# Kernel optimization log

Hardware: AMD Instinct MI355X
Metric: run time of the kernel (lower is better)

Reference implementation:

```python
import jax, jax.numpy as jnp
import numpy as np

N_NODES = 50000
N_EDGES = 500000
D_IN = 128
D_HID = 128
OUTPUT_DIM = 10.0


def gcn_conv(x, src, dst, edge_weight, W, b, n_nodes):
    # PyG GCNConv: out = D^{-1/2} (A + I) D^{-1/2} X W + b, self-loop weight 1
    xw = x @ W  # [N, D_out]
    # degree at target nodes, including self-loop weight 1
    deg = jax.ops.segment_sum(edge_weight, dst, num_segments=n_nodes) + 1.0
    dinv = jnp.where(deg > 0, jax.lax.rsqrt(deg), 0.0)  # [N]
    norm = dinv[src] * edge_weight * dinv[dst]  # [E]
    msgs = xw[src] * norm[:, None]  # [E, D_out] gathered+scaled messages
    agg = jax.ops.segment_sum(msgs, dst, num_segments=n_nodes)
    # analytic self-loop contribution: norm_ii = dinv_i * 1 * dinv_i
    agg = agg + xw * (dinv * dinv)[:, None]
    return agg + b


def setup_inputs() -> dict:
    key = jax.random.key(0)
    k = jax.random.split(key, 8)
    x = jax.random.normal(k[0], (N_NODES, D_IN), dtype=jnp.float32)
    edge_index = jax.random.randint(k[1], (2, N_EDGES), 0, N_NODES, dtype=jnp.int64)
    edge_weight = jax.random.uniform(k[2], (N_EDGES,), dtype=jnp.float32)
    s1 = 1.0 / np.sqrt(D_IN)
    s2 = 1.0 / np.sqrt(D_HID)
    W1 = jax.random.uniform(k[3], (D_IN, D_HID), minval=-s1, maxval=s1, dtype=jnp.float32)
    b1 = jnp.zeros((D_HID,), dtype=jnp.float32)
    W2 = jax.random.uniform(k[4], (D_HID, D_HID), minval=-s2, maxval=s2, dtype=jnp.float32)
    b2 = jnp.zeros((D_HID,), dtype=jnp.float32)
    Wf = jax.random.uniform(k[5], (D_HID, 1), minval=-s2, maxval=s2, dtype=jnp.float32)
    bf = jax.random.uniform(k[6], (1,), minval=-s2, maxval=s2, dtype=jnp.float32)
    return {"x": x, "edge_index": edge_index, "edge_weight": edge_weight,
            "W1": W1, "b1": b1, "W2": W2, "b2": b2, "Wf": Wf, "bf": bf}


def reference(x, edge_index, edge_weight, W1, b1, W2, b2, Wf, bf):
    src, dst = edge_index[0], edge_index[1]
    h = gcn_conv(x, src, dst, edge_weight, W1, b1, N_NODES)
    h = gcn_conv(h, src, dst, edge_weight, W2, b2, N_NODES)
    out = h @ Wf + bf  # [N, 1]
    return jax.nn.sigmoid(out) * OUTPUT_DIM
```

## Files before the change

### kernel.cpp

```cpp
#include <hip/hip_runtime.h>

#define N_NODES 50000
#define N_EDGES 500000
#define NQ (N_EDGES / 4)
#define D 128
#define NBUCK 196
#define BN 256
#define REG 4096
#define FXS 4194304.0f
#define AXS 2097152.0f

typedef unsigned long long u64;

__global__ void prep_kernel(const float* __restrict__ W1, const float* __restrict__ W2,
                            const float* __restrict__ b1, const float* __restrict__ b2,
                            const float* __restrict__ Wf, const float* __restrict__ bf,
                            float* __restrict__ v, float* __restrict__ consts,
                            unsigned* __restrict__ alloc) {
    const int t = threadIdx.x;
    if (blockIdx.x == 1) {
        if (t < 256) alloc[t] = 0u;
        return;
    }
    __shared__ float u[D];
    if (t < D) {
        float a = 0.f;
#pragma unroll 8
        for (int j = 0; j < D; ++j) a += W2[t * D + j] * Wf[j];
        u[t] = a;
    }
    __syncthreads();
    if (t < D) {
        float a = 0.f;
#pragma unroll 8
        for (int k = 0; k < D; ++k) a += W1[t * D + k] * u[k];
        v[t] = a;
    }
    if (t == 0) {
        float c = 0.f;
        for (int k = 0; k < D; ++k) c += b1[k] * u[k];
        consts[0] = c;
    } else if (t == 1) {
        float c = bf[0];
        for (int k = 0; k < D; ++k) c += b2[k] * Wf[k];
        consts[1] = c;
    }
}

__global__ __launch_bounds__(512) void bucket_kernel(const int* __restrict__ src,
                                                     const int* __restrict__ dst,
                                                     const float* __restrict__ ew,
                                                     unsigned* __restrict__ alloc,
                                                     u64* __restrict__ recs) {
    __shared__ unsigned hist[NBUCK];
    const int t = threadIdx.x;
    if (t < NBUCK) hist[t] = 0u;
    __syncthreads();
    const int q0 = blockIdx.x * 1024 + t;
    const int q1 = q0 + 512;
    int4 dA, sA, dB, sB; float4 wA, wB;
    const bool aA = q0 < NQ, aB = q1 < NQ;
    if (aA) {
        dA = ((const int4*)dst)[q0]; sA = ((const int4*)src)[q0]; wA = ((const float4*)ew)[q0];
        atomicAdd(&hist[dA.x >> 8], 1u); atomicAdd(&hist[dA.y >> 8], 1u);
        atomicAdd(&hist[dA.z >> 8], 1u); atomicAdd(&hist[dA.w >> 8], 1u);
    }
    if (aB) {
        dB = ((const int4*)dst)[q1]; sB = ((const int4*)src)[q1]; wB = ((const float4*)ew)[q1];
        atomicAdd(&hist[dB.x >> 8], 1u); atomicAdd(&hist[dB.y >> 8], 1u);
        atomicAdd(&hist[dB.z >> 8], 1u); atomicAdd(&hist[dB.w >> 8], 1u);
    }
    __syncthreads();
    if (t < NBUCK) hist[t] = atomicAdd(&alloc[t], hist[t]);
    __syncthreads();
#define PLACE(dd, ss, ww)                                                        \
    {   int bkt = (dd) >> 8;                                                     \
        unsigned p = atomicAdd(&hist[bkt], 1u);                                  \
        if (p < REG)                                                             \
            recs[(size_t)bkt * REG + p] =                                        \
                ((u64)__float_as_uint(ww) << 32) |                               \
                ((unsigned)((dd) & 255) << 16) | (unsigned)(ss);                 \
    }
    if (aA) { PLACE(dA.x, sA.x, wA.x) PLACE(dA.y, sA.y, wA.y)
              PLACE(dA.z, sA.z, wA.z) PLACE(dA.w, sA.w, wA.w) }
    if (aB) { PLACE(dB.x, sB.x, wB.x) PLACE(dB.y, sB.y, wB.y)
              PLACE(dB.z, sB.z, wB.z) PLACE(dB.w, sB.w, wB.w) }
#undef PLACE
}

__global__ void gemv_kernel(const float* __restrict__ x, const float* __restrict__ v,
                            float* __restrict__ traw) {
    __shared__ float vs[D];
    const int t = threadIdx.x;
    if (t < D) vs[t] = v[t];
    __syncthreads();
    const int l = t & 31;
    const int n = blockIdx.x * 8 + (t >> 5);
    float4 xv = ((const float4*)(x + (size_t)n * D))[l];
    float a = xv.x * vs[l * 4] + xv.y * vs[l * 4 + 1] +
              xv.z * vs[l * 4 + 2] + xv.w * vs[l * 4 + 3];
#pragma unroll
    for (int off = 16; off > 0; off >>= 1) a += __shfl_xor(a, off);
    if (l == 0) traw[n] = a;
}

__global__ __launch_bounds__(512) void degtw_kernel(const u64* __restrict__ recs,
                                                    const unsigned* __restrict__ alloc,
                                                    const float* __restrict__ traw,
                                                    float* __restrict__ dinv,
                                                    float* __restrict__ tw) {
    __shared__ unsigned ws[BN];
    const int b = blockIdx.x, t = threadIdx.x;
    if (t < BN) ws[t] = 0u;
    __syncthreads();
    unsigned total = alloc[b];
    if (total > REG) total = REG;
    const u64* rb = recs + (size_t)b * REG;
    for (unsigned i = t; i < total; i += 512) {
        u64 r = rb[i];
        float w = __uint_as_float((unsigned)(r >> 32));
        atomicAdd(&ws[((unsigned)r >> 16) & 0xffu], __float2uint_rn(w * FXS));
    }
    __syncthreads();
    if (t < BN) {
        int n = b * BN + t;
        if (n < N_NODES) {
            float di = rsqrtf((float)ws[t] * (1.0f / FXS) + 1.0f);
            dinv[n] = di;
            tw[n] = di * traw[n];
        }
    }
}

__global__ __launch_bounds__(512) void gather_s_kernel(const u64* __restrict__ recs,
                                                       const unsigned* __restrict__ alloc,
                                                       const float* __restrict__ tw,
                                                       const float* __restrict__ dinv,
                                                       const float* __restrict__ consts,
                                                       float* __restrict__ sw) {
    __shared__ int acc[BN];
    const int b = blockIdx.x, t = threadIdx.x;
    if (t < BN) acc[t] = 0;
    __syncthreads();
    unsigned total = alloc[b];
    if (total > REG) total = REG;
    const u64* rb = recs + (size_t)b * REG;
    for (unsigned i = t; i < total; i += 512) {
        u64 r = rb[i];
        unsigned lo = (unsigned)r;
        float m = __uint_as_float((unsigned)(r >> 32)) * tw[lo & 0xffffu];
        atomicAdd(&acc[(lo >> 16) & 0xffu], __float2int_rn(m * AXS));
    }
    __syncthreads();
    if (t < BN) {
        int n = b * BN + t;
        if (n < N_NODES) {
            float di = dinv[n];
            float a = (float)acc[t] * (1.0f / AXS);
            sw[n] = di * (di * (a + tw[n]) + consts[0]);
        }
    }
}

__global__ __launch_bounds__(512) void gather_z_kernel(const u64* __restrict__ recs,
                                                       const unsigned* __restrict__ alloc,
                                                       const float* __restrict__ sw,
                                                       const float* __restrict__ dinv,
                                                       const float* __restrict__ consts,
                                                       float* __restrict__ out) {
    __shared__ int acc[BN];
    const int b = blockIdx.x, t = threadIdx.x;
    if (t < BN) acc[t] = 0;
    __syncthreads();
    unsigned total = alloc[b];
    if (total > REG) total = REG;
    const u64* rb = recs + (size_t)b * REG;
    for (unsigned i = t; i < total; i += 512) {
        u64 r = rb[i];
        unsigned lo = (unsigned)r;
        float m = __uint_as_float((unsigned)(r >> 32)) * sw[lo & 0xffffu];
        atomicAdd(&acc[(lo >> 16) & 0xffu], __float2int_rn(m * AXS));
    }
    __syncthreads();
    if (t < BN) {
        int n = b * BN + t;
        if (n < N_NODES) {
            float di = dinv[n];
            float a = (float)acc[t] * (1.0f / AXS);
            float z = di * (a + sw[n]) + consts[1];
            out[n] = 10.0f / (1.0f + expf(-z));
        }
    }
}

extern "C" void kernel_launch(void* const* d_in, const int* in_sizes, int n_in,
                              void* d_out, int out_size, void* d_ws, size_t ws_size,
                              hipStream_t stream) {
    const float* x  = (const float*)d_in[0];
    const int*   ei = (const int*)d_in[1];
    const float* ew = (const float*)d_in[2];
    const float* W1 = (const float*)d_in[3];
    const float* b1 = (const float*)d_in[4];
    const float* W2 = (const float*)d_in[5];
    const float* b2 = (const float*)d_in[6];
    const float* Wf = (const float*)d_in[7];
    const float* bf = (const float*)d_in[8];
    const int* srcv = ei;
    const int* dstv = ei + N_EDGES;
    float* out = (float*)d_out;

    char* p = (char*)d_ws;
    auto alloc_ws = [&](size_t bytes) { void* r = (void*)p; p += (bytes + 255) & ~(size_t)255; return r; };
    unsigned* alloc  = (unsigned*)alloc_ws(256 * 4);
    u64*      recs   = (u64*)alloc_ws((size_t)NBUCK * REG * 8);
    float*    traw   = (float*)alloc_ws(N_NODES * 4);
    float*    dinv   = (float*)alloc_ws(N_NODES * 4);
    float*    tw     = (float*)alloc_ws(N_NODES * 4);
    float*    sw     = (float*)alloc_ws(N_NODES * 4);
    float*    v      = (float*)alloc_ws(D * 4);
    float*    consts = (float*)alloc_ws(2 * 4);

    const int BB = (NQ + 1023) / 1024;

    prep_kernel<<<2, 256, 0, stream>>>(W1, W2, b1, b2, Wf, bf, v, consts, alloc);

    bucket_kernel<<<BB, 512, 0, stream>>>(srcv, dstv, ew, alloc, recs);

    gemv_kernel<<<N_NODES / 8, 256, 0, stream>>>(x, v, traw);

    degtw_kernel<<<NBUCK, 512, 0, stream>>>(recs, alloc, traw, dinv, tw);
    gather_s_kernel<<<NBUCK, 512, 0, stream>>>(recs, alloc, tw, dinv, consts, sw);
    gather_z_kernel<<<NBUCK, 512, 0, stream>>>(recs, alloc, sw, dinv, consts, out);
}
```

Measured before the change: 118.8 us.

## Replace global-atomic bucketing with per-block cells and fuse kernels into four launches

The bucket layout changes from one global region per destination bucket, filled through global atomic offsets, to fixed 64-slot cells per (bucket, block) with per-cell counts. This removes the global alloc counters, the histogram pass and the prep launch. The prep work moves into an extra block of the build kernel, and the GEMV is merged with the degree computation into one launch. The tw buffer is dropped by computing dinv*traw inside the gather. The risk is cell overflow: edges past 64 per cell are silently dropped, which the test's random uniform distribution makes unlikely but does not rule out.

```diff
diff --git a/kernel.cpp b/kernel.cpp
--- a/kernel.cpp
+++ b/kernel.cpp
@@ -6,180 +6,188 @@
 #define D 128
 #define NBUCK 196
 #define BN 256
-#define REG 4096
+#define NBLK 123
+#define CELL 64
+#define GEMVB 3125
 #define FXS 4194304.0f
 #define AXS 2097152.0f
 
 typedef unsigned long long u64;
 
-__global__ void prep_kernel(const float* __restrict__ W1, const float* __restrict__ W2,
-                            const float* __restrict__ b1, const float* __restrict__ b2,
-                            const float* __restrict__ Wf, const float* __restrict__ bf,
-                            float* __restrict__ v, float* __restrict__ consts,
-                            unsigned* __restrict__ alloc) {
+__global__ __launch_bounds__(512) void build_kernel(const int* __restrict__ src,
+                                                    const int* __restrict__ dst,
+                                                    const float* __restrict__ ew,
+                                                    const float* __restrict__ W1,
+                                                    const float* __restrict__ W2,
+                                                    const float* __restrict__ b1,
+                                                    const float* __restrict__ b2,
+                                                    const float* __restrict__ Wf,
+                                                    const float* __restrict__ bf,
+                                                    u64* __restrict__ recs,
+                                                    unsigned* __restrict__ cnts,
+                                                    float* __restrict__ v,
+                                                    float* __restrict__ consts) {
     const int t = threadIdx.x;
-    if (blockIdx.x == 1) {
-        if (t < 256) alloc[t] = 0u;
+    const int blk = blockIdx.x;
+    if (blk == NBLK) {
+        __shared__ float u[D];
+        if (t < D) {
+            float a = 0.f;
+#pragma unroll 8
+            for (int j = 0; j < D; ++j) a += W2[t * D + j] * Wf[j];
+            u[t] = a;
+        }
+        __syncthreads();
+        if (t < D) {
+            float a = 0.f;
+#pragma unroll 8
+            for (int k = 0; k < D; ++k) a += W1[t * D + k] * u[k];
+            v[t] = a;
+        }
+        if (t == 0) {
+            float c = 0.f;
+            for (int k = 0; k < D; ++k) c += b1[k] * u[k];
+            consts[0] = c;
+        } else if (t == 1) {
+            float c = bf[0];
+            for (int k = 0; k < D; ++k) c += b2[k] * Wf[k];
+            consts[1] = c;
+        }
         return;
     }
-    __shared__ float u[D];
-    if (t < D) {
-        float a = 0.f;
-#pragma unroll 8
-        for (int j = 0; j < D; ++j) a += W2[t * D + j] * Wf[j];
-        u[t] = a;
-    }
-    __syncthreads();
-    if (t < D) {
-        float a = 0.f;
-#pragma unroll 8
-        for (int k = 0; k < D; ++k) a += W1[t * D + k] * u[k];
-        v[t] = a;
-    }
-    if (t == 0) {
-        float c = 0.f;
-        for (int k = 0; k < D; ++k) c += b1[k] * u[k];
-        consts[0] = c;
-    } else if (t == 1) {
-        float c = bf[0];
-        for (int k = 0; k < D; ++k) c += b2[k] * Wf[k];
-        consts[1] = c;
-    }
-}
-
-__global__ __launch_bounds__(512) void bucket_kernel(const int* __restrict__ src,
-                                                     const int* __restrict__ dst,
-                                                     const float* __restrict__ ew,
-                                                     unsigned* __restrict__ alloc,
-                                                     u64* __restrict__ recs) {
-    __shared__ unsigned hist[NBUCK];
+    __shared__ unsigned cur[NBUCK];
+    if (t < NBUCK) cur[t] = 0u;
+    __syncthreads();
+    const int q0 = blk * 1024 + t;
+    const int q1 = q0 + 512;
+#define PLACE(dd, ss, ww)                                                         \
+    {   int bkt = (dd) >> 8;                                                      \
+        unsigned slot = atomicAdd(&cur[bkt], 1u);                                 \
+        if (slot < CELL)                                                          \
+            recs[((size_t)bkt * NBLK + blk) * CELL + slot] =                      \
+                ((u64)__float_as_uint(ww) << 32) |                                \
+                ((unsigned)((dd) & 255) << 16) | (unsigned)(ss);                  \
+    }
+    if (q0 < NQ) {
+        int4 d4 = ((const int4*)dst)[q0];
+        int4 s4 = ((const int4*)src)[q0];
+        float4 w4 = ((const float4*)ew)[q0];
+        PLACE(d4.x, s4.x, w4.x) PLACE(d4.y, s4.y, w4.y)
+        PLACE(d4.z, s4.z, w4.z) PLACE(d4.w, s4.w, w4.w)
+    }
+    if (q1 < NQ) {
+        int4 d4 = ((const int4*)dst)[q1];
+        int4 s4 = ((const int4*)src)[q1];
+        float4 w4 = ((const float4*)ew)[q1];
+        PLACE(d4.x, s4.x, w4.x) PLACE(d4.y, s4.y, w4.y)
+        PLACE(d4.z, s4.z, w4.z) PLACE(d4.w, s4.w, w4.w)
+    }
+#undef PLACE
+    __syncthreads();
+    if (t < NBUCK) {
+        unsigned c = cur[t];
+        cnts[(size_t)t * NBLK + blk] = (c < CELL) ? c : CELL;
+    }
+}
+
+__global__ __launch_bounds__(512) void mid_kernel(const float* __restrict__ x,
+                                                  const float* __restrict__ v,
+                                                  const u64* __restrict__ recs,
+                                                  const unsigned* __restrict__ cnts,
+                                                  float* __restrict__ traw,
+                                                  float* __restrict__ dinv) {
     const int t = threadIdx.x;
-    if (t < NBUCK) hist[t] = 0u;
-    __syncthreads();
-    const int q0 = blockIdx.x * 1024 + t;
-    const int q1 = q0 + 512;
-    int4 dA, sA, dB, sB; float4 wA, wB;
-    const bool aA = q0 < NQ, aB = q1 < NQ;
-    if (aA) {
-        dA = ((const int4*)dst)[q0]; sA = ((const int4*)src)[q0]; wA = ((const float4*)ew)[q0];
-        atomicAdd(&hist[dA.x >> 8], 1u); atomicAdd(&hist[dA.y >> 8], 1u);
-        atomicAdd(&hist[dA.z >> 8], 1u); atomicAdd(&hist[dA.w >> 8], 1u);
-    }
-    if (aB) {
-        dB = ((const int4*)dst)[q1]; sB = ((const int4*)src)[q1]; wB = ((const float4*)ew)[q1];
-        atomicAdd(&hist[dB.x >> 8], 1u); atomicAdd(&hist[dB.y >> 8], 1u);
-        atomicAdd(&hist[dB.z >> 8], 1u); atomicAdd(&hist[dB.w >> 8], 1u);
-    }
-    __syncthreads();
-    if (t < NBUCK) hist[t] = atomicAdd(&alloc[t], hist[t]);
-    __syncthreads();
-#define PLACE(dd, ss, ww)                                                        \
-    {   int bkt = (dd) >> 8;                                                     \
-        unsigned p = atomicAdd(&hist[bkt], 1u);                                  \
-        if (p < REG)                                                             \
-            recs[(size_t)bkt * REG + p] =                                        \
-                ((u64)__float_as_uint(ww) << 32) |                               \
-                ((unsigned)((dd) & 255) << 16) | (unsigned)(ss);                 \
-    }
-    if (aA) { PLACE(dA.x, sA.x, wA.x) PLACE(dA.y, sA.y, wA.y)
-              PLACE(dA.z, sA.z, wA.z) PLACE(dA.w, sA.w, wA.w) }
-    if (aB) { PLACE(dB.x, sB.x, wB.x) PLACE(dB.y, sB.y, wB.y)
-              PLACE(dB.z, sB.z, wB.z) PLACE(dB.w, sB.w, wB.w) }
-#undef PLACE
-}
-
-__global__ void gemv_kernel(const float* __restrict__ x, const float* __restrict__ v,
-                            float* __restrict__ traw) {
-    __shared__ float vs[D];
-    const int t = threadIdx.x;
-    if (t < D) vs[t] = v[t];
-    __syncthreads();
-    const int l = t & 31;
-    const int n = blockIdx.x * 8 + (t >> 5);
-    float4 xv = ((const float4*)(x + (size_t)n * D))[l];
-    float a = xv.x * vs[l * 4] + xv.y * vs[l * 4 + 1] +
-              xv.z * vs[l * 4 + 2] + xv.w * vs[l * 4 + 3];
+    const int bid = blockIdx.x;
+    if (bid < GEMVB) {
+        __shared__ float vs[D];
+        if (t < D) vs[t] = v[t];
+        __syncthreads();
+        const int l = t & 31;
+        const int n = bid * 16 + (t >> 5);
+        float4 xv = ((const float4*)(x + (size_t)n * D))[l];
+        float a = xv.x * vs[l * 4] + xv.y * vs[l * 4 + 1] +
+                  xv.z * vs[l * 4 + 2] + xv.w * vs[l * 4 + 3];
 #pragma unroll
-    for (int off = 16; off > 0; off >>= 1) a += __shfl_xor(a, off);
-    if (l == 0) traw[n] = a;
-}
-
-__global__ __launch_bounds__(512) void degtw_kernel(const u64* __restrict__ recs,
-                                                    const unsigned* __restrict__ alloc,
-                                                    const float* __restrict__ traw,
-                                                    float* __restrict__ dinv,
-                                                    float* __restrict__ tw) {
+        for (int off = 16; off > 0; off >>= 1) a += __shfl_xor(a, off);
+        if (l == 0) traw[n] = a;
+        return;
+    }
+    const int b = bid - GEMVB;
     __shared__ unsigned ws[BN];
-    const int b = blockIdx.x, t = threadIdx.x;
+    __shared__ unsigned cl[NBLK];
     if (t < BN) ws[t] = 0u;
-    __syncthreads();
-    unsigned total = alloc[b];
-    if (total > REG) total = REG;
-    const u64* rb = recs + (size_t)b * REG;
-    for (unsigned i = t; i < total; i += 512) {
-        u64 r = rb[i];
-        float w = __uint_as_float((unsigned)(r >> 32));
-        atomicAdd(&ws[((unsigned)r >> 16) & 0xffu], __float2uint_rn(w * FXS));
+    if (t < NBLK) cl[t] = cnts[(size_t)b * NBLK + t];
+    __syncthreads();
+    const int wid = t >> 6, lane = t & 63;
+    for (int c = wid; c < NBLK; c += 8) {
+        if (lane < (int)cl[c]) {
+            u64 r = recs[((size_t)b * NBLK + c) * CELL + lane];
+            float w = __uint_as_float((unsigned)(r >> 32));
+            atomicAdd(&ws[((unsigned)r >> 16) & 0xffu], __float2uint_rn(w * FXS));
+        }
     }
     __syncthreads();
     if (t < BN) {
         int n = b * BN + t;
-        if (n < N_NODES) {
-            float di = rsqrtf((float)ws[t] * (1.0f / FXS) + 1.0f);
-            dinv[n] = di;
-            tw[n] = di * traw[n];
-        }
+        if (n < N_NODES)
+            dinv[n] = rsqrtf((float)ws[t] * (1.0f / FXS) + 1.0f);
     }
 }
 
 __global__ __launch_bounds__(512) void gather_s_kernel(const u64* __restrict__ recs,
-                                                       const unsigned* __restrict__ alloc,
-                                                       const float* __restrict__ tw,
+                                                       const unsigned* __restrict__ cnts,
+                                                       const float* __restrict__ traw,
                                                        const float* __restrict__ dinv,
                                                        const float* __restrict__ consts,
                                                        float* __restrict__ sw) {
+    const int b = blockIdx.x, t = threadIdx.x;
     __shared__ int acc[BN];
-    const int b = blockIdx.x, t = threadIdx.x;
+    __shared__ unsigned cl[NBLK];
     if (t < BN) acc[t] = 0;
-    __syncthreads();
-    unsigned total = alloc[b];
-    if (total > REG) total = REG;
-    const u64* rb = recs + (size_t)b * REG;
-    for (unsigned i = t; i < total; i += 512) {
-        u64 r = rb[i];
-        unsigned lo = (unsigned)r;
-        float m = __uint_as_float((unsigned)(r >> 32)) * tw[lo & 0xffffu];
-        atomicAdd(&acc[(lo >> 16) & 0xffu], __float2int_rn(m * AXS));
+    if (t < NBLK) cl[t] = cnts[(size_t)b * NBLK + t];
+    __syncthreads();
+    const int wid = t >> 6, lane = t & 63;
+    for (int c = wid; c < NBLK; c += 8) {
+        if (lane < (int)cl[c]) {
+            u64 r = recs[((size_t)b * NBLK + c) * CELL + lane];
+            unsigned lo = (unsigned)r;
+            int s = lo & 0xffff;
+            float m = __uint_as_float((unsigned)(r >> 32)) * dinv[s] * traw[s];
+            atomicAdd(&acc[(lo >> 16) & 0xffu], __float2int_rn(m * AXS));
+        }
     }
     __syncthreads();
     if (t < BN) {
         int n = b * BN + t;
         if (n < N_NODES) {
             float di = dinv[n];
+            float twn = di * traw[n];
             float a = (float)acc[t] * (1.0f / AXS);
-            sw[n] = di * (di * (a + tw[n]) + consts[0]);
+            sw[n] = di * (di * (a + twn) + consts[0]);
         }
     }
 }
 
 __global__ __launch_bounds__(512) void gather_z_kernel(const u64* __restrict__ recs,
-                                                       const unsigned* __restrict__ alloc,
+                                                       const unsigned* __restrict__ cnts,
                                                        const float* __restrict__ sw,
                                                        const float* __restrict__ dinv,
                                                        const float* __restrict__ consts,
                                                        float* __restrict__ out) {
+    const int b = blockIdx.x, t = threadIdx.x;
     __shared__ int acc[BN];
-    const int b = blockIdx.x, t = threadIdx.x;
+    __shared__ unsigned cl[NBLK];
     if (t < BN) acc[t] = 0;
-    __syncthreads();
-    unsigned total = alloc[b];
-    if (total > REG) total = REG;
-    const u64* rb = recs + (size_t)b * REG;
-    for (unsigned i = t; i < total; i += 512) {
-        u64 r = rb[i];
-        unsigned lo = (unsigned)r;
-        float m = __uint_as_float((unsigned)(r >> 32)) * sw[lo & 0xffffu];
-        atomicAdd(&acc[(lo >> 16) & 0xffu], __float2int_rn(m * AXS));
+    if (t < NBLK) cl[t] = cnts[(size_t)b * NBLK + t];
+    __syncthreads();
+    const int wid = t >> 6, lane = t & 63;
+    for (int c = wid; c < NBLK; c += 8) {
+        if (lane < (int)cl[c]) {
+            u64 r = recs[((size_t)b * NBLK + c) * CELL + lane];
+            unsigned lo = (unsigned)r;
+            float m = __uint_as_float((unsigned)(r >> 32)) * sw[lo & 0xffffu];
+            atomicAdd(&acc[(lo >> 16) & 0xffu], __float2int_rn(m * AXS));
+        }
     }
     __syncthreads();
     if (t < BN) {
@@ -211,24 +219,19 @@
 
     char* p = (char*)d_ws;
     auto alloc_ws = [&](size_t bytes) { void* r = (void*)p; p += (bytes + 255) & ~(size_t)255; return r; };
-    unsigned* alloc  = (unsigned*)alloc_ws(256 * 4);
-    u64*      recs   = (u64*)alloc_ws((size_t)NBUCK * REG * 8);
+    u64*      recs   = (u64*)alloc_ws((size_t)NBUCK * NBLK * CELL * 8);
+    unsigned* cnts   = (unsigned*)alloc_ws((size_t)NBUCK * NBLK * 4);
     float*    traw   = (float*)alloc_ws(N_NODES * 4);
     float*    dinv   = (float*)alloc_ws(N_NODES * 4);
-    float*    tw     = (float*)alloc_ws(N_NODES * 4);
     float*    sw     = (float*)alloc_ws(N_NODES * 4);
     float*    v      = (float*)alloc_ws(D * 4);
     float*    consts = (float*)alloc_ws(2 * 4);
 
-    const int BB = (NQ + 1023) / 1024;
-
-    prep_kernel<<<2, 256, 0, stream>>>(W1, W2, b1, b2, Wf, bf, v, consts, alloc);
-
-    bucket_kernel<<<BB, 512, 0, stream>>>(srcv, dstv, ew, alloc, recs);
-
-    gemv_kernel<<<N_NODES / 8, 256, 0, stream>>>(x, v, traw);
-
-    degtw_kernel<<<NBUCK, 512, 0, stream>>>(recs, alloc, traw, dinv, tw);
-    gather_s_kernel<<<NBUCK, 512, 0, stream>>>(recs, alloc, tw, dinv, consts, sw);
-    gather_z_kernel<<<NBUCK, 512, 0, stream>>>(recs, alloc, sw, dinv, consts, out);
-}
+    build_kernel<<<NBLK + 1, 512, 0, stream>>>(srcv, dstv, ew, W1, W2, b1, b2, Wf, bf,
+                                               recs, cnts, v, consts);
+
+    mid_kernel<<<GEMVB + NBUCK, 512, 0, stream>>>(x, v, recs, cnts, traw, dinv);
+
+    gather_s_kernel<<<NBUCK, 512, 0, stream>>>(recs, cnts, traw, dinv, consts, sw);
+    gather_z_kernel<<<NBUCK, 512, 0, stream>>>(recs, cnts, sw, dinv, consts, out);
+}
```

Measured after the change: 120.6 us. No clear change (+1.5%).

## Merge prep into bucket kernel and gemv with degree pass to cut launches

Applied to the files above, without the earlier changes.

Moves the weight-folding prep work into an extra block of the bucketing kernel and replaces the alloc zeroing with a memset. The gemv and degree computation now run as independent block ranges of one kernel, and the tw array is dropped, so the gather recomputes dinv*traw per edge. The intent is to remove kernel launches and their serialization gaps in a launch-bound pipeline, at the cost of an extra gather per edge in gather_s.

```diff
diff --git a/kernel.cpp b/kernel.cpp
--- a/kernel.cpp
+++ b/kernel.cpp
@@ -7,53 +7,54 @@
 #define NBUCK 196
 #define BN 256
 #define REG 4096
+#define GEMVB 3125
 #define FXS 4194304.0f
 #define AXS 2097152.0f
 
 typedef unsigned long long u64;
-
-__global__ void prep_kernel(const float* __restrict__ W1, const float* __restrict__ W2,
-                            const float* __restrict__ b1, const float* __restrict__ b2,
-                            const float* __restrict__ Wf, const float* __restrict__ bf,
-                            float* __restrict__ v, float* __restrict__ consts,
-                            unsigned* __restrict__ alloc) {
-    const int t = threadIdx.x;
-    if (blockIdx.x == 1) {
-        if (t < 256) alloc[t] = 0u;
-        return;
-    }
-    __shared__ float u[D];
-    if (t < D) {
-        float a = 0.f;
-#pragma unroll 8
-        for (int j = 0; j < D; ++j) a += W2[t * D + j] * Wf[j];
-        u[t] = a;
-    }
-    __syncthreads();
-    if (t < D) {
-        float a = 0.f;
-#pragma unroll 8
-        for (int k = 0; k < D; ++k) a += W1[t * D + k] * u[k];
-        v[t] = a;
-    }
-    if (t == 0) {
-        float c = 0.f;
-        for (int k = 0; k < D; ++k) c += b1[k] * u[k];
-        consts[0] = c;
-    } else if (t == 1) {
-        float c = bf[0];
-        for (int k = 0; k < D; ++k) c += b2[k] * Wf[k];
-        consts[1] = c;
-    }
-}
 
 __global__ __launch_bounds__(512) void bucket_kernel(const int* __restrict__ src,
                                                      const int* __restrict__ dst,
                                                      const float* __restrict__ ew,
+                                                     const float* __restrict__ W1,
+                                                     const float* __restrict__ W2,
+                                                     const float* __restrict__ b1,
+                                                     const float* __restrict__ b2,
+                                                     const float* __restrict__ Wf,
+                                                     const float* __restrict__ bf,
                                                      unsigned* __restrict__ alloc,
-                                                     u64* __restrict__ recs) {
+                                                     u64* __restrict__ recs,
+                                                     float* __restrict__ v,
+                                                     float* __restrict__ consts,
+                                                     int nwb) {
+    const int t = threadIdx.x;
+    if ((int)blockIdx.x == nwb) {
+        __shared__ float u[D];
+        if (t < D) {
+            float a = 0.f;
+#pragma unroll 8
+            for (int j = 0; j < D; ++j) a += W2[t * D + j] * Wf[j];
+            u[t] = a;
+        }
+        __syncthreads();
+        if (t < D) {
+            float a = 0.f;
+#pragma unroll 8
+            for (int k = 0; k < D; ++k) a += W1[t * D + k] * u[k];
+            v[t] = a;
+        }
+        if (t == 0) {
+            float c = 0.f;
+            for (int k = 0; k < D; ++k) c += b1[k] * u[k];
+            consts[0] = c;
+        } else if (t == 1) {
+            float c = bf[0];
+            for (int k = 0; k < D; ++k) c += b2[k] * Wf[k];
+            consts[1] = c;
+        }
+        return;
+    }
     __shared__ unsigned hist[NBUCK];
-    const int t = threadIdx.x;
     if (t < NBUCK) hist[t] = 0u;
     __syncthreads();
     const int q0 = blockIdx.x * 1024 + t;
@@ -88,29 +89,30 @@
 #undef PLACE
 }
 
-__global__ void gemv_kernel(const float* __restrict__ x, const float* __restrict__ v,
-                            float* __restrict__ traw) {
-    __shared__ float vs[D];
+__global__ __launch_bounds__(512) void mid_kernel(const float* __restrict__ x,
+                                                  const float* __restrict__ v,
+                                                  const u64* __restrict__ recs,
+                                                  const unsigned* __restrict__ alloc,
+                                                  float* __restrict__ traw,
+                                                  float* __restrict__ dinv) {
     const int t = threadIdx.x;
-    if (t < D) vs[t] = v[t];
-    __syncthreads();
-    const int l = t & 31;
-    const int n = blockIdx.x * 8 + (t >> 5);
-    float4 xv = ((const float4*)(x + (size_t)n * D))[l];
-    float a = xv.x * vs[l * 4] + xv.y * vs[l * 4 + 1] +
-              xv.z * vs[l * 4 + 2] + xv.w * vs[l * 4 + 3];
+    const int bid = blockIdx.x;
+    if (bid < GEMVB) {
+        __shared__ float vs[D];
+        if (t < D) vs[t] = v[t];
+        __syncthreads();
+        const int l = t & 31;
+        const int n = bid * 16 + (t >> 5);
+        float4 xv = ((const float4*)(x + (size_t)n * D))[l];
+        float a = xv.x * vs[l * 4] + xv.y * vs[l * 4 + 1] +
+                  xv.z * vs[l * 4 + 2] + xv.w * vs[l * 4 + 3];
 #pragma unroll
-    for (int off = 16; off > 0; off >>= 1) a += __shfl_xor(a, off);
-    if (l == 0) traw[n] = a;
-}
-
-__global__ __launch_bounds__(512) void degtw_kernel(const u64* __restrict__ recs,
-                                                    const unsigned* __restrict__ alloc,
-                                                    const float* __restrict__ traw,
-                                                    float* __restrict__ dinv,
-                                                    float* __restrict__ tw) {
+        for (int off = 16; off > 0; off >>= 1) a += __shfl_xor(a, off);
+        if (l == 0) traw[n] = a;
+        return;
+    }
+    const int b = bid - GEMVB;
     __shared__ unsigned ws[BN];
-    const int b = blockIdx.x, t = threadIdx.x;
     if (t < BN) ws[t] = 0u;
     __syncthreads();
     unsigned total = alloc[b];
@@ -124,17 +126,14 @@
     __syncthreads();
     if (t < BN) {
         int n = b * BN + t;
-        if (n < N_NODES) {
-            float di = rsqrtf((float)ws[t] * (1.0f / FXS) + 1.0f);
-            dinv[n] = di;
-            tw[n] = di * traw[n];
-        }
+        if (n < N_NODES)
+            dinv[n] = rsqrtf((float)ws[t] * (1.0f / FXS) + 1.0f);
     }
 }
 
 __global__ __launch_bounds__(512) void gather_s_kernel(const u64* __restrict__ recs,
                                                        const unsigned* __restrict__ alloc,
-                                                       const float* __restrict__ tw,
+                                                       const float* __restrict__ traw,
                                                        const float* __restrict__ dinv,
                                                        const float* __restrict__ consts,
                                                        float* __restrict__ sw) {
@@ -148,7 +147,8 @@
     for (unsigned i = t; i < total; i += 512) {
         u64 r = rb[i];
         unsigned lo = (unsigned)r;
-        float m = __uint_as_float((unsigned)(r >> 32)) * tw[lo & 0xffffu];
+        int s = lo & 0xffff;
+        float m = __uint_as_float((unsigned)(r >> 32)) * dinv[s] * traw[s];
         atomicAdd(&acc[(lo >> 16) & 0xffu], __float2int_rn(m * AXS));
     }
     __syncthreads();
@@ -156,8 +156,9 @@
         int n = b * BN + t;
         if (n < N_NODES) {
             float di = dinv[n];
+            float twn = di * traw[n];
             float a = (float)acc[t] * (1.0f / AXS);
-            sw[n] = di * (di * (a + tw[n]) + consts[0]);
+            sw[n] = di * (di * (a + twn) + consts[0]);
         }
     }
 }
@@ -215,20 +216,19 @@
     u64*      recs   = (u64*)alloc_ws((size_t)NBUCK * REG * 8);
     float*    traw   = (float*)alloc_ws(N_NODES * 4);
     float*    dinv   = (float*)alloc_ws(N_NODES * 4);
-    float*    tw     = (float*)alloc_ws(N_NODES * 4);
     float*    sw     = (float*)alloc_ws(N_NODES * 4);
     float*    v      = (float*)alloc_ws(D * 4);
     float*    consts = (float*)alloc_ws(2 * 4);
 
-    const int BB = (NQ + 1023) / 1024;
-
-    prep_kernel<<<2, 256, 0, stream>>>(W1, W2, b1, b2, Wf, bf, v, consts, alloc);
-
-    bucket_kernel<<<BB, 512, 0, stream>>>(srcv, dstv, ew, alloc, recs);
-
-    gemv_kernel<<<N_NODES / 8, 256, 0, stream>>>(x, v, traw);
-
-    degtw_kernel<<<NBUCK, 512, 0, stream>>>(recs, alloc, traw, dinv, tw);
-    gather_s_kernel<<<NBUCK, 512, 0, stream>>>(recs, alloc, tw, dinv, consts, sw);
+    const int NWB = (NQ + 1023) / 1024;
+
+    hipMemsetAsync(alloc, 0, NBUCK * 4, stream);
+
+    bucket_kernel<<<NWB + 1, 512, 0, stream>>>(srcv, dstv, ew, W1, W2, b1, b2, Wf, bf,
+                                               alloc, recs, v, consts, NWB);
+
+    mid_kernel<<<GEMVB + NBUCK, 512, 0, stream>>>(x, v, recs, alloc, traw, dinv);
+
+    gather_s_kernel<<<NBUCK, 512, 0, stream>>>(recs, alloc, traw, dinv, consts, sw);
     gather_z_kernel<<<NBUCK, 512, 0, stream>>>(recs, alloc, sw, dinv, consts, out);
 }
```

Measured after the change: 114.3 us, median of 2. -3.8%, faster.
